# Kernel optimization log

Measured on AMD Instinct MI355X. Metric: run time of the kernel, lower is better.

Reference implementation:

```python
import jax, jax.numpy as jnp
import numpy as np

POOLED = 7          # output_size (7x7 bins)
SPATIAL_SCALE = 0.0625  # 1/16 backbone stride


def setup_inputs() -> dict:
    key = jax.random.key(0)
    k1, k2, k3, k4 = jax.random.split(key, 4)
    B, C, H, W = 4, 1029, 80, 80   # C = output_dim(21) * 7 * 7
    N = 1024                        # number of ROIs
    x = jax.random.normal(k1, (B, C, H, W), dtype=jnp.float32)
    img_w = W / SPATIAL_SCALE       # 1280 px
    img_h = H / SPATIAL_SCALE
    bidx = jax.random.randint(k2, (N,), 0, B).astype(jnp.float32)
    xs = jax.random.uniform(k3, (N, 2), dtype=jnp.float32) * img_w
    ys = jax.random.uniform(k4, (N, 2), dtype=jnp.float32) * img_h
    x1 = jnp.min(xs, axis=1); x2 = jnp.max(xs, axis=1)
    y1 = jnp.min(ys, axis=1); y2 = jnp.max(ys, axis=1)
    rois = jnp.stack([bidx, x1, y1, x2, y2], axis=1)  # [N,5]
    return {"input": x, "rois": rois}


def reference(input, rois):
    # Position-sensitive ROI average pooling (R-FCN / Caffe semantics).
    B, C, H, W = input.shape
    Ph = Pw = POOLED
    D = C // (Ph * Pw)  # output_dim
    N = rois.shape[0]

    # Summed-area table so each bin average is 4 gathers (same math as
    # summing the bin then dividing by its area). Padded with a zero row/col.
    sat = jnp.cumsum(jnp.cumsum(input, axis=2), axis=3)
    sat = jnp.pad(sat, ((0, 0), (0, 0), (1, 0), (1, 0)))

    b = rois[:, 0].astype(jnp.int32)
    rnd = lambda v: jnp.floor(v + 0.5)  # C round() for non-negative coords
    roi_sw = rnd(rois[:, 1]) * SPATIAL_SCALE
    roi_sh = rnd(rois[:, 2]) * SPATIAL_SCALE
    roi_ew = rnd(rois[:, 3] + 1.0) * SPATIAL_SCALE
    roi_eh = rnd(rois[:, 4] + 1.0) * SPATIAL_SCALE
    roi_w = jnp.maximum(roi_ew - roi_sw, 0.1)
    roi_h = jnp.maximum(roi_eh - roi_sh, 0.1)
    bin_h = roi_h / Ph  # [N]
    bin_w = roi_w / Pw

    ph = jnp.arange(Ph, dtype=jnp.float32)
    pw = jnp.arange(Pw, dtype=jnp.float32)
    hs = jnp.clip(jnp.floor(ph[None, :] * bin_h[:, None] + roi_sh[:, None]), 0, H).astype(jnp.int32)   # [N,Ph]
    he = jnp.clip(jnp.ceil((ph[None, :] + 1.0) * bin_h[:, None] + roi_sh[:, None]), 0, H).astype(jnp.int32)
    ws = jnp.clip(jnp.floor(pw[None, :] * bin_w[:, None] + roi_sw[:, None]), 0, W).astype(jnp.int32)   # [N,Pw]
    we = jnp.clip(jnp.ceil((pw[None, :] + 1.0) * bin_w[:, None] + roi_sw[:, None]), 0, W).astype(jnp.int32)

    # position-sensitive channel: c = (d*Ph + ph)*Pw + pw  -> [D,Ph,Pw]
    c = (jnp.arange(D)[:, None, None] * Ph + jnp.arange(Ph)[None, :, None]) * Pw + jnp.arange(Pw)[None, None, :]

    bI = b[:, None, None, None]          # [N,1,1,1]
    cI = c[None, :, :, :]                # [1,D,Ph,Pw]
    hsI = hs[:, None, :, None]; heI = he[:, None, :, None]  # [N,1,Ph,1]
    wsI = ws[:, None, None, :]; weI = we[:, None, None, :]  # [N,1,1,Pw]

    s = (sat[bI, cI, heI, weI] - sat[bI, cI, hsI, weI]
         - sat[bI, cI, heI, wsI] + sat[bI, cI, hsI, wsI])   # [N,D,Ph,Pw]

    area = ((he - hs)[:, None, :, None] * (we - ws)[:, None, None, :]).astype(input.dtype)
    out = jnp.where(area > 0, s / jnp.maximum(area, 1.0), jnp.zeros((), input.dtype))
    return out  # [N, D, Ph, Pw]
```

## Files before the change

kernel.cpp:

```cpp
#include <hip/hip_runtime.h>
#include <stdint.h>


#define PSB 4
#define PSC 1029
#define PSH 80
#define PSW 80
#define PSCALE 0.0625f
#define PLANE_ELEMS (PSH * PSW)
#define NROI_MAX 1024

#define WS_COUNTS 0
#define WS_LISTS  16
#define WS_HTAB   (16 + 4 * NROI_MAX * 4)
#define WS_WTAB   (WS_HTAB + NROI_MAX * 7 * 2)

typedef __attribute__((address_space(3))) void lds_void;
typedef __attribute__((address_space(1))) void glob_void;

__global__ __launch_bounds__(256) void psroi_prep_kernel(
    const float* __restrict__ rois, int N,
    int* __restrict__ counts, int* __restrict__ lists,
    uint16_t* __restrict__ hTab, uint16_t* __restrict__ wTab)
{
    int n = blockIdx.x * blockDim.x + threadIdx.x;
    if (n >= N) return;

    const float* r = rois + (size_t)n * 5;
    int   b      = (int)r[0];
    float roi_sw = floorf(r[1] + 0.5f) * PSCALE;
    float roi_sh = floorf(r[2] + 0.5f) * PSCALE;
    float roi_ew = floorf(r[3] + 1.5f) * PSCALE;
    float roi_eh = floorf(r[4] + 1.5f) * PSCALE;

    float roi_w = fmaxf(roi_ew - roi_sw, 0.1f);
    float roi_h = fmaxf(roi_eh - roi_sh, 0.1f);
    float bin_h = roi_h * (1.0f / 7.0f);
    float bin_w = roi_w * (1.0f / 7.0f);

    #pragma unroll
    for (int p = 0; p < 7; ++p) {
        float fp = (float)p;
        int hs = (int)fminf(fmaxf(floorf(fp * bin_h + roi_sh), 0.0f), (float)PSH);
        int he = (int)fminf(fmaxf(ceilf((fp + 1.0f) * bin_h + roi_sh), 0.0f), (float)PSH);
        int ws = (int)fminf(fmaxf(floorf(fp * bin_w + roi_sw), 0.0f), (float)PSW);
        int we = (int)fminf(fmaxf(ceilf((fp + 1.0f) * bin_w + roi_sw), 0.0f), (float)PSW);
        hTab[n * 7 + p] = (uint16_t)(hs | (he << 8));
        wTab[n * 7 + p] = (uint16_t)(ws | (we << 8));
    }

    int slot = atomicAdd(&counts[b], 1);
    lists[b * NROI_MAX + slot] = n;
}

__global__ __launch_bounds__(256) void psroi_main_kernel(
    const float* __restrict__ x,
    float* __restrict__ out,
    const int* __restrict__ counts,
    const int* __restrict__ lists,
    const uint16_t* __restrict__ hTab,
    const uint16_t* __restrict__ wTab)
{
    const int blk = blockIdx.x;
    const int b   = blk / PSC;
    const int c   = blk - b * PSC;
    const int ph  = (c / 7) % 7;
    const int pw  = c % 7;

    __shared__ float plane[PLANE_ELEMS];

    {
        const float4* src4 = (const float4*)(x + ((size_t)b * PSC + c) * PLANE_ELEMS);
        float4* dst4 = (float4*)plane;
        int tid = threadIdx.x;
        #pragma unroll
        for (int i = 0; i < 6; ++i) {
            __builtin_amdgcn_global_load_lds(
                (const glob_void*)(src4 + tid + i * 256),
                (lds_void*)(dst4 + tid + i * 256), 16, 0, 0);
        }
        if (tid < 64) {
            __builtin_amdgcn_global_load_lds(
                (const glob_void*)(src4 + tid + 1536),
                (lds_void*)(dst4 + tid + 1536), 16, 0, 0);
        }
    }
    __syncthreads();

    const int cnt = counts[b];
    const int* list = lists + b * NROI_MAX;

    for (int i = threadIdx.x; i < cnt; i += 256) {
        int n  = list[i];
        int hr = hTab[n * 7 + ph];
        int wr = wTab[n * 7 + pw];
        int hs = hr & 0xFF, he = hr >> 8;
        int ws = wr & 0xFF, we = wr >> 8;

        float s = 0.0f;
        for (int h = hs; h < he; ++h) {
            const float* row = plane + h * PSW;
            for (int w = ws; w < we; ++w) s += row[w];
        }

        int area = (he - hs) * (we - ws);
        out[(size_t)n * PSC + c] = (area > 0) ? s / (float)area : 0.0f;
    }
}

extern "C" void kernel_launch(void* const* d_in, const int* in_sizes, int n_in,
                              void* d_out, int out_size, void* d_ws, size_t ws_size,
                              hipStream_t stream) {
    const float* x    = (const float*)d_in[0];
    const float* rois = (const float*)d_in[1];
    float* out        = (float*)d_out;
    int N = in_sizes[1] / 5;

    char* ws = (char*)d_ws;
    int*      counts = (int*)(ws + WS_COUNTS);
    int*      lists  = (int*)(ws + WS_LISTS);
    uint16_t* hTab   = (uint16_t*)(ws + WS_HTAB);
    uint16_t* wTab   = (uint16_t*)(ws + WS_WTAB);

    hipMemsetAsync(counts, 0, 4 * sizeof(int), stream);
    psroi_prep_kernel<<<(N + 255) / 256, 256, 0, stream>>>(
        rois, N, counts, lists, hTab, wTab);
    psroi_main_kernel<<<PSB * PSC, 256, 0, stream>>>(
        x, out, counts, lists, hTab, wTab);
}
```

Baseline: 175.0 us.

## Sort ROIs by batch and bin size, write transposed output, add transpose kernel

The prep kernel now runs as one 1024-thread block. It counting-sorts ROIs by batch and by a coarse bin-size class, so threads in a wavefront get similar loop trip counts, and it stores the per-slot tables in sorted order. The main kernel writes results channel-major into a workspace buffer indexed by sorted slot, which makes stores coalesced instead of strided by PSC. A new tiled transpose kernel scatters those results back to the [N, C] output through the sorted list. The cost is an extra kernel launch plus an extra read and write of the whole output. The code also assumes N <= 1024 and N a multiple of 32.

Result: no change. 171.8 us (-1.9%).

```diff
diff --git a/kernel.cpp b/kernel.cpp
--- a/kernel.cpp
+++ b/kernel.cpp
@@ -8,56 +8,97 @@
 #define PSW 80
 #define PSCALE 0.0625f
 #define PLANE_ELEMS (PSH * PSW)
-#define NROI_MAX 1024
-
-#define WS_COUNTS 0
-#define WS_LISTS  16
-#define WS_HTAB   (16 + 4 * NROI_MAX * 4)
-#define WS_WTAB   (WS_HTAB + NROI_MAX * 7 * 2)
+#define NMAX 1024
+#define NCLASS 32
+#define NKEYS (PSB * NCLASS)
+
+#define WS_OFF  0
+#define WS_LIST 32
+#define WS_HTAB (WS_LIST + NMAX * 4)
+#define WS_WTAB (WS_HTAB + NMAX * 7 * 2)
+#define WS_OUTT 65536
 
 typedef __attribute__((address_space(3))) void lds_void;
 typedef __attribute__((address_space(1))) void glob_void;
 
-__global__ __launch_bounds__(256) void psroi_prep_kernel(
+__global__ __launch_bounds__(1024) void psroi_prep(
     const float* __restrict__ rois, int N,
-    int* __restrict__ counts, int* __restrict__ lists,
+    int* __restrict__ off_g, int* __restrict__ list,
     uint16_t* __restrict__ hTab, uint16_t* __restrict__ wTab)
 {
-    int n = blockIdx.x * blockDim.x + threadIdx.x;
-    if (n >= N) return;
-
-    const float* r = rois + (size_t)n * 5;
-    int   b      = (int)r[0];
-    float roi_sw = floorf(r[1] + 0.5f) * PSCALE;
-    float roi_sh = floorf(r[2] + 0.5f) * PSCALE;
-    float roi_ew = floorf(r[3] + 1.5f) * PSCALE;
-    float roi_eh = floorf(r[4] + 1.5f) * PSCALE;
-
-    float roi_w = fmaxf(roi_ew - roi_sw, 0.1f);
-    float roi_h = fmaxf(roi_eh - roi_sh, 0.1f);
-    float bin_h = roi_h * (1.0f / 7.0f);
-    float bin_w = roi_w * (1.0f / 7.0f);
-
-    #pragma unroll
-    for (int p = 0; p < 7; ++p) {
-        float fp = (float)p;
-        int hs = (int)fminf(fmaxf(floorf(fp * bin_h + roi_sh), 0.0f), (float)PSH);
-        int he = (int)fminf(fmaxf(ceilf((fp + 1.0f) * bin_h + roi_sh), 0.0f), (float)PSH);
-        int ws = (int)fminf(fmaxf(floorf(fp * bin_w + roi_sw), 0.0f), (float)PSW);
-        int we = (int)fminf(fmaxf(ceilf((fp + 1.0f) * bin_w + roi_sw), 0.0f), (float)PSW);
-        hTab[n * 7 + p] = (uint16_t)(hs | (he << 8));
-        wTab[n * 7 + p] = (uint16_t)(ws | (we << 8));
-    }
-
-    int slot = atomicAdd(&counts[b], 1);
-    lists[b * NROI_MAX + slot] = n;
-}
-
-__global__ __launch_bounds__(256) void psroi_main_kernel(
+    __shared__ int hist[NKEYS];
+    __shared__ int scan[NKEYS];
+    __shared__ int cur[NKEYS];
+
+    const int tid = threadIdx.x;
+    if (tid < NKEYS) hist[tid] = 0;
+    __syncthreads();
+
+    const bool act = tid < N;
+    int key = 0;
+    uint16_t hr[7], wr[7];
+
+    if (act) {
+        const float* r = rois + (size_t)tid * 5;
+        int   b      = (int)r[0];
+        float roi_sw = floorf(r[1] + 0.5f) * PSCALE;
+        float roi_sh = floorf(r[2] + 0.5f) * PSCALE;
+        float roi_ew = floorf(r[3] + 1.5f) * PSCALE;
+        float roi_eh = floorf(r[4] + 1.5f) * PSCALE;
+
+        float roi_w = fmaxf(roi_ew - roi_sw, 0.1f);
+        float roi_h = fmaxf(roi_eh - roi_sh, 0.1f);
+        float bin_h = roi_h * (1.0f / 7.0f);
+        float bin_w = roi_w * (1.0f / 7.0f);
+
+        #pragma unroll
+        for (int p = 0; p < 7; ++p) {
+            float fp = (float)p;
+            int hs = (int)fminf(fmaxf(floorf(fp * bin_h + roi_sh), 0.0f), (float)PSH);
+            int he = (int)fminf(fmaxf(ceilf((fp + 1.0f) * bin_h + roi_sh), 0.0f), (float)PSH);
+            int ws = (int)fminf(fmaxf(floorf(fp * bin_w + roi_sw), 0.0f), (float)PSW);
+            int we = (int)fminf(fmaxf(ceilf((fp + 1.0f) * bin_w + roi_sw), 0.0f), (float)PSW);
+            hr[p] = (uint16_t)(hs | (he << 8));
+            wr[p] = (uint16_t)(ws | (we << 8));
+        }
+
+        int kh = min(7, (int)bin_h);
+        int kw = min(3, (int)(bin_w * 0.75f));
+        key = b * NCLASS + kh * 4 + kw;
+        atomicAdd(&hist[key], 1);
+    }
+    __syncthreads();
+
+    if (tid < NKEYS) scan[tid] = hist[tid];
+    __syncthreads();
+    for (int o = 1; o < NKEYS; o <<= 1) {
+        int t = 0;
+        if (tid < NKEYS && tid >= o) t = scan[tid - o];
+        __syncthreads();
+        if (tid < NKEYS) scan[tid] += t;
+        __syncthreads();
+    }
+
+    if (tid < NKEYS) cur[tid] = scan[tid] - hist[tid];
+    if (tid < PSB)   off_g[tid] = scan[tid * NCLASS] - hist[tid * NCLASS];
+    if (tid == 0)    off_g[PSB] = N;
+    __syncthreads();
+
+    if (act) {
+        int slot = atomicAdd(&cur[key], 1);
+        list[slot] = tid;
+        #pragma unroll
+        for (int p = 0; p < 7; ++p) {
+            hTab[slot * 7 + p] = hr[p];
+            wTab[slot * 7 + p] = wr[p];
+        }
+    }
+}
+
+__global__ __launch_bounds__(256) void psroi_main(
     const float* __restrict__ x,
-    float* __restrict__ out,
-    const int* __restrict__ counts,
-    const int* __restrict__ lists,
+    float* __restrict__ outT,
+    const int* __restrict__ off_g,
     const uint16_t* __restrict__ hTab,
     const uint16_t* __restrict__ wTab)
 {
@@ -87,13 +128,12 @@
     }
     __syncthreads();
 
-    const int cnt = counts[b];
-    const int* list = lists + b * NROI_MAX;
-
-    for (int i = threadIdx.x; i < cnt; i += 256) {
-        int n  = list[i];
-        int hr = hTab[n * 7 + ph];
-        int wr = wTab[n * 7 + pw];
+    const int s0 = off_g[b];
+    const int s1 = off_g[b + 1];
+
+    for (int i = s0 + (int)threadIdx.x; i < s1; i += 256) {
+        int hr = hTab[i * 7 + ph];
+        int wr = wTab[i * 7 + pw];
         int hs = hr & 0xFF, he = hr >> 8;
         int ws = wr & 0xFF, we = wr >> 8;
 
@@ -104,7 +144,39 @@
         }
 
         int area = (he - hs) * (we - ws);
-        out[(size_t)n * PSC + c] = (area > 0) ? s / (float)area : 0.0f;
+        outT[(size_t)c * NMAX + i] = (area > 0) ? s / (float)area : 0.0f;
+    }
+}
+
+__global__ __launch_bounds__(256) void psroi_transpose(
+    const float* __restrict__ outT,
+    const int* __restrict__ list,
+    float* __restrict__ out)
+{
+    __shared__ float tile[32][33];
+    __shared__ int ntab[32];
+
+    const int c0 = blockIdx.x * 32;
+    const int s0 = blockIdx.y * 32;
+    const int tid = threadIdx.x;
+
+    if (tid < 32) ntab[tid] = list[s0 + tid];
+
+    #pragma unroll
+    for (int k = 0; k < 4; ++k) {
+        int idx = tid + k * 256;
+        int r = idx >> 5, s = idx & 31;
+        int c = c0 + r;
+        if (c < PSC) tile[r][s] = outT[(size_t)c * NMAX + s0 + s];
+    }
+    __syncthreads();
+
+    #pragma unroll
+    for (int k = 0; k < 4; ++k) {
+        int idx = tid + k * 256;
+        int j = idx >> 5, cc = idx & 31;
+        int c = c0 + cc;
+        if (c < PSC) out[(size_t)ntab[j] * PSC + c] = tile[cc][j];
     }
 }
 
@@ -117,14 +189,14 @@
     int N = in_sizes[1] / 5;
 
     char* ws = (char*)d_ws;
-    int*      counts = (int*)(ws + WS_COUNTS);
-    int*      lists  = (int*)(ws + WS_LISTS);
-    uint16_t* hTab   = (uint16_t*)(ws + WS_HTAB);
-    uint16_t* wTab   = (uint16_t*)(ws + WS_WTAB);
-
-    hipMemsetAsync(counts, 0, 4 * sizeof(int), stream);
-    psroi_prep_kernel<<<(N + 255) / 256, 256, 0, stream>>>(
-        rois, N, counts, lists, hTab, wTab);
-    psroi_main_kernel<<<PSB * PSC, 256, 0, stream>>>(
-        x, out, counts, lists, hTab, wTab);
-}
+    int*      off_g = (int*)(ws + WS_OFF);
+    int*      list  = (int*)(ws + WS_LIST);
+    uint16_t* hTab  = (uint16_t*)(ws + WS_HTAB);
+    uint16_t* wTab  = (uint16_t*)(ws + WS_WTAB);
+    float*    outT  = (float*)(ws + WS_OUTT);
+
+    psroi_prep<<<1, 1024, 0, stream>>>(rois, N, off_g, list, hTab, wTab);
+    psroi_main<<<PSB * PSC, 256, 0, stream>>>(x, outT, off_g, hTab, wTab);
+    psroi_transpose<<<dim3((PSC + 31) / 32, N / 32), 256, 0, stream>>>(
+        outT, list, out);
+}
```
